# Optimization experiments

Measured on AMD Instinct MI355X. Metric: run time of the kernel, lower is better.

Reference implementation:

```python
import jax, jax.numpy as jnp
import numpy as np

HIDDEN = 50
INPUT = 4

def setup_inputs() -> dict:
    key = jax.random.key(0)
    ks = jax.random.split(key, 7)
    B, T = 4096, 512
    s_ih = 1.0 / np.sqrt(HIDDEN)
    return {
        "x": jax.random.normal(ks[0], (B, T, INPUT), dtype=jnp.float32),
        "W_ih": jax.random.uniform(ks[1], (4 * HIDDEN, INPUT), jnp.float32, -s_ih, s_ih),
        "W_hh": jax.random.uniform(ks[2], (4 * HIDDEN, HIDDEN), jnp.float32, -s_ih, s_ih),
        "b_ih": jax.random.uniform(ks[3], (4 * HIDDEN,), jnp.float32, -s_ih, s_ih),
        "b_hh": jax.random.uniform(ks[4], (4 * HIDDEN,), jnp.float32, -s_ih, s_ih),
        "W_fc": jax.random.uniform(ks[5], (1, HIDDEN), jnp.float32, -s_ih, s_ih),
        "b_fc": jax.random.uniform(ks[6], (1,), jnp.float32, -s_ih, s_ih),
    }

def reference(x, W_ih, W_hh, b_ih, b_hh, W_fc, b_fc):
    B = x.shape[0]
    b = b_ih + b_hh  # fold biases once
    # precompute input projection for all timesteps: [B,T,4H]
    x_proj = jnp.einsum('btd,gd->btg', x, W_ih) + b
    h0 = jnp.zeros((B, HIDDEN), x.dtype)
    c0 = jnp.zeros((B, HIDDEN), x.dtype)

    def step(carry, xp_t):
        h, c = carry
        gates = xp_t + h @ W_hh.T  # [B,4H]
        i, f, g, o = jnp.split(gates, 4, axis=-1)  # PyTorch gate order i,f,g,o
        i = jax.nn.sigmoid(i)
        f = jax.nn.sigmoid(f)
        g = jnp.tanh(g)
        o = jax.nn.sigmoid(o)
        c_new = f * c + i * g
        h_new = o * jnp.tanh(c_new)
        return (h_new, c_new), None

    (h_T, _), _ = jax.lax.scan(step, (h0, c0), jnp.swapaxes(x_proj, 0, 1))
    # fc applied to last timestep only (out[:, -1, :])
    return h_T @ W_fc.T + b_fc  # [B,1]
```

## Files before the change

### kernel.cpp

```cpp
#include <hip/hip_runtime.h>


#define HID  50
#define NROW 200
#define TT   512
#define NIN  4
#define BT   16
#define KD   72
#define XOFF 56
#define NW   8

typedef float f32x4 __attribute__((ext_vector_type(4)));
typedef short s16x8 __attribute__((ext_vector_type(8)));

__device__ __forceinline__ unsigned short f2bf(float f) {
    unsigned u = __builtin_bit_cast(unsigned, f);
    return (unsigned short)((u + 0x7FFF + ((u >> 16) & 1)) >> 16);
}
__device__ __forceinline__ float fast_sigmoid(float v) {
    float e = __builtin_amdgcn_exp2f(v * -1.442695040888963f);
    return __builtin_amdgcn_rcpf(1.0f + e);
}
__device__ __forceinline__ float fast_tanh(float v) {
    float e = __builtin_amdgcn_exp2f(v * -2.885390081777927f);
    return 2.0f * __builtin_amdgcn_rcpf(1.0f + e) - 1.0f;
}

__global__ __launch_bounds__(64 * NW, 2)
void lstm_mfma(const float* __restrict__ x,
               const float* __restrict__ W_ih,
               const float* __restrict__ W_hh,
               const float* __restrict__ b_ih,
               const float* __restrict__ b_hh,
               const float* __restrict__ W_fc,
               const float* __restrict__ b_fc,
               float* __restrict__ out)
{
    __shared__ __align__(16) unsigned short buf[2][BT][KD];
    __shared__ float red[BT];

    const int tid = threadIdx.x;
    const int w   = tid >> 6;
    const int l   = tid & 63;
    const int lr  = l & 15;
    const int lg  = l >> 4;
    const int b0  = blockIdx.x * BT;

    for (int i = tid; i < 2 * BT * KD; i += 64 * NW)
        ((unsigned short*)buf)[i] = 0;
    if (tid < BT) red[tid] = 0.0f;

    s16x8 afrag[2][2];
    f32x4 bias[2];
    float wfc[2];
#pragma unroll
    for (int ti = 0; ti < 2; ++ti) {
        const int T   = w + 8 * ti;
        const int row = 16 * T + lr;
        const int u   = row >> 2, g = row & 3;
        const bool real = row < NROW;
#pragma unroll
        for (int kh = 0; kh < 2; ++kh) {
            s16x8 f;
#pragma unroll
            for (int j = 0; j < 8; ++j) {
                const int k = 32 * kh + 8 * lg + j;
                float v = 0.0f;
                if (real) {
                    if (k < HID)                        v = W_hh[(g * HID + u) * HID + k];
                    else if (k >= XOFF && k < XOFF+NIN) v = W_ih[(g * HID + u) * NIN + (k - XOFF)];
                }
                f[j] = (short)f2bf(v);
            }
            afrag[ti][kh] = f;
        }
        f32x4 bv;
#pragma unroll
        for (int r = 0; r < 4; ++r) {
            const int rr = 16 * T + 4 * lg + r;
            bv[r] = (rr < NROW) ? (b_ih[(rr & 3) * HID + (rr >> 2)] +
                                   b_hh[(rr & 3) * HID + (rr >> 2)]) : 0.0f;
        }
        bias[ti] = bv;
        const int uu = 4 * T + lg;
        wfc[ti] = (uu < HID) ? W_fc[uu] : 0.0f;
    }

    const float* xb = x + (size_t)(b0 + lr) * TT * NIN;
    if (w == 7 && l < 16) {
        const float4 xv = *(const float4*)xb;
        uint2 pk;
        pk.x = (unsigned)f2bf(xv.x) | ((unsigned)f2bf(xv.y) << 16);
        pk.y = (unsigned)f2bf(xv.z) | ((unsigned)f2bf(xv.w) << 16);
        *(uint2*)&buf[0][lr][XOFF] = pk;
    }
    __syncthreads();

    float c[2]  = {0.0f, 0.0f};
    float hr[2] = {0.0f, 0.0f};

    for (int t = 0; t < TT; ++t) {
        const int p = t & 1;

        float4 xv;
        const bool xduty = (w == 7) && (l < 16) && (t + 1 < TT);
        if (xduty) xv = *(const float4*)(xb + (size_t)(t + 1) * NIN);

        const s16x8 bf0 = *(const s16x8*)&buf[p][lr][8 * lg];
        const s16x8 bf1 = *(const s16x8*)&buf[p][lr][32 + 8 * lg];

        f32x4 acc0 = bias[0], acc1 = bias[1];
        acc0 = __builtin_amdgcn_mfma_f32_16x16x32_bf16(afrag[0][0], bf0, acc0, 0, 0, 0);
        acc0 = __builtin_amdgcn_mfma_f32_16x16x32_bf16(afrag[0][1], bf1, acc0, 0, 0, 0);
        acc1 = __builtin_amdgcn_mfma_f32_16x16x32_bf16(afrag[1][0], bf0, acc1, 0, 0, 0);
        acc1 = __builtin_amdgcn_mfma_f32_16x16x32_bf16(afrag[1][1], bf1, acc1, 0, 0, 0);

        if (xduty) {
            uint2 pk;
            pk.x = (unsigned)f2bf(xv.x) | ((unsigned)f2bf(xv.y) << 16);
            pk.y = (unsigned)f2bf(xv.z) | ((unsigned)f2bf(xv.w) << 16);
            *(uint2*)&buf[p ^ 1][lr][XOFF] = pk;
        }

#pragma unroll
        for (int ti = 0; ti < 2; ++ti) {
            const f32x4 a = ti ? acc1 : acc0;
            const float gi = fast_sigmoid(a[0]);
            const float gf = fast_sigmoid(a[1]);
            const float gg = fast_tanh(a[2]);
            const float go = fast_sigmoid(a[3]);
            c[ti] = gf * c[ti] + gi * gg;
            const float h = go * fast_tanh(c[ti]);
            hr[ti] = h;
            const int u = 4 * (w + 8 * ti) + lg;
            if (u < HID) buf[p ^ 1][lr][u] = f2bf(h);
        }
        __syncthreads();
    }

    float partial = wfc[0] * hr[0] + wfc[1] * hr[1];
    partial += __shfl_down(partial, 32);
    partial += __shfl_down(partial, 16);
    if (l < 16) atomicAdd(&red[l], partial);
    __syncthreads();
    if (tid < BT) out[b0 + tid] = red[tid] + b_fc[0];
}

extern "C" void kernel_launch(void* const* d_in, const int* in_sizes, int n_in,
                              void* d_out, int out_size, void* d_ws, size_t ws_size,
                              hipStream_t stream) {
    const float* x    = (const float*)d_in[0];
    const float* W_ih = (const float*)d_in[1];
    const float* W_hh = (const float*)d_in[2];
    const float* b_ih = (const float*)d_in[3];
    const float* b_hh = (const float*)d_in[4];
    const float* W_fc = (const float*)d_in[5];
    const float* b_fc = (const float*)d_in[6];
    float* out        = (float*)d_out;

    const int B = in_sizes[0] / (TT * NIN);
    lstm_mfma<<<B / BT, 64 * NW, 0, stream>>>(x, W_ih, W_hh, b_ih, b_hh, W_fc, b_fc, out);
}
```

Measured before the change: 300.8 us.

## Assign only real gate tiles to waves and permute hidden-state K layout

The original assigned 16 row-tiles across 8 waves, two each, although only 13 tiles (200 rows) are real, so 3 tiles of MFMA and activation work were wasted. The new mapping gives waves 0-4 two tiles and waves 5-7 one tile, skipping the padded tiles. The K dimension of the hidden-state buffer is permuted so each wave's two h outputs can be packed with a single bf16 convert. The x input is now loaded as one scalar per lane at slot 13 of each 16-wide group instead of a float4 packed by 16 lanes. Waves are now unbalanced (some do half the work), and the critical path per step may still be set by the two-tile waves.

```diff
diff --git a/kernel.cpp b/kernel.cpp
--- a/kernel.cpp
+++ b/kernel.cpp
@@ -7,7 +7,6 @@
 #define NIN  4
 #define BT   16
 #define KD   72
-#define XOFF 56
 #define NW   8
 
 typedef float f32x4 __attribute__((ext_vector_type(4)));
@@ -26,15 +25,26 @@
     return 2.0f * __builtin_amdgcn_rcpf(1.0f + e) - 1.0f;
 }
 
+__device__ __forceinline__ float wval(const float* W_hh, const float* W_ih,
+                                      int rowp, int k) {
+    if (rowp >= NROW) return 0.0f;
+    const int ur = rowp >> 2, g = rowp & 3;
+    const int a = k >> 4, b = k & 15;
+    if (b <= 12) { const int u = 4 * b + a;
+                   return (u < HID) ? W_hh[(g * HID + ur) * HID + u] : 0.0f; }
+    if (b == 13) return W_ih[(g * HID + ur) * NIN + a];
+    return 0.0f;
+}
+
 __global__ __launch_bounds__(64 * NW, 2)
-void lstm_mfma(const float* __restrict__ x,
-               const float* __restrict__ W_ih,
-               const float* __restrict__ W_hh,
-               const float* __restrict__ b_ih,
-               const float* __restrict__ b_hh,
-               const float* __restrict__ W_fc,
-               const float* __restrict__ b_fc,
-               float* __restrict__ out)
+void lstm_mfma3(const float* __restrict__ x,
+                const float* __restrict__ W_ih,
+                const float* __restrict__ W_hh,
+                const float* __restrict__ b_ih,
+                const float* __restrict__ b_hh,
+                const float* __restrict__ W_fc,
+                const float* __restrict__ b_fc,
+                float* __restrict__ out)
 {
     __shared__ __align__(16) unsigned short buf[2][BT][KD];
     __shared__ float red[BT];
@@ -50,95 +60,106 @@
         ((unsigned short*)buf)[i] = 0;
     if (tid < BT) red[tid] = 0.0f;
 
-    s16x8 afrag[2][2];
-    f32x4 bias[2];
-    float wfc[2];
-#pragma unroll
-    for (int ti = 0; ti < 2; ++ti) {
-        const int T   = w + 8 * ti;
-        const int row = 16 * T + lr;
-        const int u   = row >> 2, g = row & 3;
-        const bool real = row < NROW;
+    const bool two = (w < 5);
+    const int  T0  = two ? w : (w + 5);
+    const int  T1  = w + 5;
+
+    s16x8 af0[2], af1[2];
+    f32x4 bias0, bias1 = {0.f, 0.f, 0.f, 0.f};
+    float wfc0 = 0.0f, wfc1 = 0.0f;
+    {
+        const int rowp = 16 * T0 + lr;
 #pragma unroll
         for (int kh = 0; kh < 2; ++kh) {
             s16x8 f;
 #pragma unroll
-            for (int j = 0; j < 8; ++j) {
-                const int k = 32 * kh + 8 * lg + j;
-                float v = 0.0f;
-                if (real) {
-                    if (k < HID)                        v = W_hh[(g * HID + u) * HID + k];
-                    else if (k >= XOFF && k < XOFF+NIN) v = W_ih[(g * HID + u) * NIN + (k - XOFF)];
-                }
-                f[j] = (short)f2bf(v);
-            }
-            afrag[ti][kh] = f;
+            for (int j = 0; j < 8; ++j)
+                f[j] = (short)f2bf(wval(W_hh, W_ih, rowp, 32 * kh + 8 * lg + j));
+            af0[kh] = f;
         }
-        f32x4 bv;
 #pragma unroll
         for (int r = 0; r < 4; ++r) {
-            const int rr = 16 * T + 4 * lg + r;
-            bv[r] = (rr < NROW) ? (b_ih[(rr & 3) * HID + (rr >> 2)] +
-                                   b_hh[(rr & 3) * HID + (rr >> 2)]) : 0.0f;
+            const int rr = 16 * T0 + 4 * lg + r;
+            bias0[r] = (rr < NROW) ? (b_ih[(rr & 3) * HID + (rr >> 2)] +
+                                      b_hh[(rr & 3) * HID + (rr >> 2)]) : 0.0f;
         }
-        bias[ti] = bv;
-        const int uu = 4 * T + lg;
-        wfc[ti] = (uu < HID) ? W_fc[uu] : 0.0f;
+        const int u = 4 * T0 + lg;
+        wfc0 = (u < HID) ? W_fc[u] : 0.0f;
+    }
+    if (two) {
+        const int rowp = 16 * T1 + lr;
+#pragma unroll
+        for (int kh = 0; kh < 2; ++kh) {
+            s16x8 f;
+#pragma unroll
+            for (int j = 0; j < 8; ++j)
+                f[j] = (short)f2bf(wval(W_hh, W_ih, rowp, 32 * kh + 8 * lg + j));
+            af1[kh] = f;
+        }
+#pragma unroll
+        for (int r = 0; r < 4; ++r) {
+            const int rr = 16 * T1 + 4 * lg + r;
+            bias1[r] = (rr < NROW) ? (b_ih[(rr & 3) * HID + (rr >> 2)] +
+                                      b_hh[(rr & 3) * HID + (rr >> 2)]) : 0.0f;
+        }
+        const int u = 4 * T1 + lg;
+        wfc1 = (u < HID) ? W_fc[u] : 0.0f;
     }
 
-    const float* xb = x + (size_t)(b0 + lr) * TT * NIN;
-    if (w == 7 && l < 16) {
-        const float4 xv = *(const float4*)xb;
-        uint2 pk;
-        pk.x = (unsigned)f2bf(xv.x) | ((unsigned)f2bf(xv.y) << 16);
-        pk.y = (unsigned)f2bf(xv.z) | ((unsigned)f2bf(xv.w) << 16);
-        *(uint2*)&buf[0][lr][XOFF] = pk;
-    }
+    const float* xg = x + ((size_t)(b0 + lr) * TT) * NIN + lg;
+    if (w == 7) buf[0][lr][16 * lg + 13] = f2bf(xg[0]);
     __syncthreads();
 
-    float c[2]  = {0.0f, 0.0f};
-    float hr[2] = {0.0f, 0.0f};
+    float c0 = 0.f, h0 = 0.f, c1 = 0.f, h1 = 0.f;
 
     for (int t = 0; t < TT; ++t) {
         const int p = t & 1;
 
-        float4 xv;
-        const bool xduty = (w == 7) && (l < 16) && (t + 1 < TT);
-        if (xduty) xv = *(const float4*)(xb + (size_t)(t + 1) * NIN);
+        float xv = 0.0f;
+        const bool xload = (w == 7) && (t + 1 < TT);
+        if (xload) xv = xg[(size_t)(t + 1) * NIN];
 
-        const s16x8 bf0 = *(const s16x8*)&buf[p][lr][8 * lg];
-        const s16x8 bf1 = *(const s16x8*)&buf[p][lr][32 + 8 * lg];
+        const s16x8 bf0v = *(const s16x8*)&buf[p][lr][8 * lg];
+        const s16x8 bf1v = *(const s16x8*)&buf[p][lr][32 + 8 * lg];
 
-        f32x4 acc0 = bias[0], acc1 = bias[1];
-        acc0 = __builtin_amdgcn_mfma_f32_16x16x32_bf16(afrag[0][0], bf0, acc0, 0, 0, 0);
-        acc0 = __builtin_amdgcn_mfma_f32_16x16x32_bf16(afrag[0][1], bf1, acc0, 0, 0, 0);
-        acc1 = __builtin_amdgcn_mfma_f32_16x16x32_bf16(afrag[1][0], bf0, acc1, 0, 0, 0);
-        acc1 = __builtin_amdgcn_mfma_f32_16x16x32_bf16(afrag[1][1], bf1, acc1, 0, 0, 0);
-
-        if (xduty) {
-            uint2 pk;
-            pk.x = (unsigned)f2bf(xv.x) | ((unsigned)f2bf(xv.y) << 16);
-            pk.y = (unsigned)f2bf(xv.z) | ((unsigned)f2bf(xv.w) << 16);
-            *(uint2*)&buf[p ^ 1][lr][XOFF] = pk;
+        f32x4 a0 = bias0;
+        a0 = __builtin_amdgcn_mfma_f32_16x16x32_bf16(af0[0], bf0v, a0, 0, 0, 0);
+        a0 = __builtin_amdgcn_mfma_f32_16x16x32_bf16(af0[1], bf1v, a0, 0, 0, 0);
+        f32x4 a1;
+        if (two) {
+            a1 = bias1;
+            a1 = __builtin_amdgcn_mfma_f32_16x16x32_bf16(af1[0], bf0v, a1, 0, 0, 0);
+            a1 = __builtin_amdgcn_mfma_f32_16x16x32_bf16(af1[1], bf1v, a1, 0, 0, 0);
         }
 
-#pragma unroll
-        for (int ti = 0; ti < 2; ++ti) {
-            const f32x4 a = ti ? acc1 : acc0;
-            const float gi = fast_sigmoid(a[0]);
-            const float gf = fast_sigmoid(a[1]);
-            const float gg = fast_tanh(a[2]);
-            const float go = fast_sigmoid(a[3]);
-            c[ti] = gf * c[ti] + gi * gg;
-            const float h = go * fast_tanh(c[ti]);
-            hr[ti] = h;
-            const int u = 4 * (w + 8 * ti) + lg;
-            if (u < HID) buf[p ^ 1][lr][u] = f2bf(h);
+        if (xload) buf[p ^ 1][lr][16 * lg + 13] = f2bf(xv);
+
+        {
+            const float gi = fast_sigmoid(a0[0]);
+            const float gf = fast_sigmoid(a0[1]);
+            const float gg = fast_tanh(a0[2]);
+            const float go = fast_sigmoid(a0[3]);
+            c0 = gf * c0 + gi * gg;
+            h0 = go * fast_tanh(c0);
+        }
+        if (two) {
+            const float gi = fast_sigmoid(a1[0]);
+            const float gf = fast_sigmoid(a1[1]);
+            const float gg = fast_tanh(a1[2]);
+            const float go = fast_sigmoid(a1[3]);
+            c1 = gf * c1 + gi * gg;
+            h1 = go * fast_tanh(c1);
+            unsigned pk;
+            asm("v_cvt_pk_bf16_f32 %0, %1, %2" : "=v"(pk) : "v"(h0), "v"(h1));
+            buf[p ^ 1][lr][16 * lg + T0] = (unsigned short)pk;
+            buf[p ^ 1][lr][16 * lg + T1] = (unsigned short)(pk >> 16);
+        } else {
+            buf[p ^ 1][lr][16 * lg + T0] = f2bf(h0);
         }
         __syncthreads();
     }
 
-    float partial = wfc[0] * hr[0] + wfc[1] * hr[1];
+    float partial = wfc0 * h0 + wfc1 * h1;
     partial += __shfl_down(partial, 32);
     partial += __shfl_down(partial, 16);
     if (l < 16) atomicAdd(&red[l], partial);
@@ -159,5 +180,5 @@
     float* out        = (float*)d_out;
 
     const int B = in_sizes[0] / (TT * NIN);
-    lstm_mfma<<<B / BT, 64 * NW, 0, stream>>>(x, W_ih, W_hh, b_ih, b_hh, W_fc, b_fc, out);
+    lstm_mfma3<<<B / BT, 64 * NW, 0, stream>>>(x, W_ih, W_hh, b_ih, b_hh, W_fc, b_fc, out);
 }
```

New measurement: 303.8 us. Within noise of the previous version (+1.0%).
